# Kernel tuning notes

Hardware: AMD Instinct MI355X
Metric: run time of the kernel (lower is better)

Reference implementation:

```python
import jax, jax.numpy as jnp
import numpy as np

D_MODEL = 1024
NUM_HEADS = 16
HEAD_DIM = D_MODEL // NUM_HEADS
THETA = 10000.0


def _rope(x):
    # x: [B, H, S, Dk]; interleaved even/odd rotation as in the torch module
    *_, seq_len, d_k = x.shape
    d = d_k // 2
    inv_freq = 1.0 / (THETA ** (2.0 * jnp.arange(d, dtype=jnp.float32) / d_k))
    pos = jnp.arange(seq_len, dtype=jnp.float32)
    angles = pos[:, None] * inv_freq[None, :]  # [S, d]
    cos = jnp.cos(angles)
    sin = jnp.sin(angles)
    x_even = x[..., 0::2]
    x_odd = x[..., 1::2]
    rot_even = x_even * cos - x_odd * sin
    rot_odd = x_even * sin + x_odd * cos
    return jnp.stack([rot_even, rot_odd], axis=-1).reshape(x.shape)


def setup_inputs() -> dict:
    key = jax.random.key(0)
    ks = jax.random.split(key, 5)
    B, S = 4, 2048
    x = jax.random.normal(ks[0], (B, S, D_MODEL), dtype=jnp.float32)
    q_w = jax.random.uniform(ks[1], (D_MODEL, D_MODEL), dtype=jnp.float32)
    k_w = jax.random.uniform(ks[2], (D_MODEL, D_MODEL), dtype=jnp.float32)
    v_w = jax.random.uniform(ks[3], (D_MODEL, D_MODEL), dtype=jnp.float32)
    o_w = jax.random.uniform(ks[4], (D_MODEL, D_MODEL), dtype=jnp.float32)
    return {"x": x, "q_w": q_w, "k_w": k_w, "v_w": v_w, "o_w": o_w}


def reference(x, q_w, k_w, v_w, o_w):
    B, S, _ = x.shape
    def split_heads(t):
        return t.reshape(B, S, NUM_HEADS, HEAD_DIM).transpose(0, 2, 1, 3)  # [B,H,S,Dk]
    Q = split_heads(x @ q_w.T)
    K = split_heads(x @ k_w.T)
    V = split_heads(x @ v_w.T)
    Q = _rope(Q)
    K = _rope(K)
    scale = 1.0 / jnp.sqrt(jnp.float32(HEAD_DIM))
    scores = jnp.einsum('bhqd,bhkd->bhqk', Q, K) * scale  # [B,H,S,S]
    causal = jnp.tril(jnp.ones((S, S), dtype=bool))
    scores = jnp.where(causal[None, None], scores, -jnp.inf)
    attn = jax.nn.softmax(scores, axis=-1)
    out = jnp.einsum('bhqk,bhkd->bhqd', attn, V)  # [B,H,S,Dk]
    out = out.transpose(0, 2, 1, 3).reshape(B, S, D_MODEL)
    return out @ o_w.T
```

## Files before the change

### kernel.cpp

```cpp
#include <hip/hip_runtime.h>
#include <hip/hip_bf16.h>
#include <cstdint>
#include <cstddef>

#define D_MODEL   1024
#define NUM_HEADS 16
#define HEAD_DIM  64
#define SEQ       2048
#define BATCH     4
#define BH        (BATCH*NUM_HEADS)
#define MROWS     (BATCH*SEQ)

typedef _Float16 half8  __attribute__((ext_vector_type(8)));
typedef _Float16 half4v __attribute__((ext_vector_type(4)));
typedef float    floatx4 __attribute__((ext_vector_type(4)));

__device__ inline void gld_lds16(const void* g, void* l) {
    __builtin_amdgcn_global_load_lds(
        (__attribute__((address_space(1))) void*)g,
        (__attribute__((address_space(3))) void*)l,
        16, 0, 0);
}

__global__ void rope_table(float2* __restrict__ tab) {
    const int i = blockIdx.x * blockDim.x + threadIdx.x;
    const int p = i & 31, s = i >> 5;
    const double inv = pow(10000.0, -(double)p / 32.0);
    const double ang = (double)s * inv;
    tab[i] = make_float2((float)cos(ang), (float)sin(ang));
}

__global__ void f32_split_f16(const float* __restrict__ in,
                              _Float16* __restrict__ hi,
                              _Float16* __restrict__ lo, int n4) {
    int i = blockIdx.x * blockDim.x + threadIdx.x;
    if (i >= n4) return;
    float4 v = ((const float4*)in)[i];
    half4v h = { (_Float16)v.x, (_Float16)v.y, (_Float16)v.z, (_Float16)v.w };
    half4v l = { (_Float16)(v.x - (float)h.x), (_Float16)(v.y - (float)h.y),
                 (_Float16)(v.z - (float)h.z), (_Float16)(v.w - (float)h.w) };
    ((half4v*)hi)[i] = h;
    ((half4v*)lo)[i] = l;
}

__global__ void conv_weights(const float* __restrict__ qw, const float* __restrict__ kw,
                             const float* __restrict__ vw, const float* __restrict__ ow,
                             _Float16* __restrict__ qwh, _Float16* __restrict__ qwl,
                             _Float16* __restrict__ kwh, _Float16* __restrict__ kwl,
                             _Float16* __restrict__ vwh, _Float16* __restrict__ owh) {
    const int i = blockIdx.x * blockDim.x + threadIdx.x;
    const int which = i >> 18;
    const int j = i & 262143;
    const float4 v = ((const float4*)(which == 0 ? qw : which == 1 ? kw :
                                      which == 2 ? vw : ow))[j];
    half4v h = { (_Float16)v.x, (_Float16)v.y, (_Float16)v.z, (_Float16)v.w };
    if (which < 2) {
        half4v l = { (_Float16)(v.x - (float)h.x), (_Float16)(v.y - (float)h.y),
                     (_Float16)(v.z - (float)h.z), (_Float16)(v.w - (float)h.w) };
        ((half4v*)(which ? kwh : qwh))[j] = h;
        ((half4v*)(which ? kwl : qwl))[j] = l;
    } else {
        ((half4v*)(which == 2 ? vwh : owh))[j] = h;
    }
}

__global__ __launch_bounds__(256)
void gemm_bt(const _Float16* __restrict__ A, const _Float16* __restrict__ B,
             float* __restrict__ Cout, int M, int N, int K) {
    __shared__ _Float16 AB[2][2][128*32];

    const int nb  = N >> 7;
    const int nwg = gridDim.x;
    int lb = blockIdx.x;
    if ((nwg & 7) == 0)
        lb = (blockIdx.x & 7) * (nwg >> 3) + (blockIdx.x >> 3);
    const int bx = lb % nb;
    const int by = lb / nb;
    const int m0 = by << 7, n0 = bx << 7;

    const int t    = threadIdx.x;
    const int w    = t >> 6;
    const int lane = t & 63;
    const int r    = lane & 15;
    const int quad = lane >> 4;
    const int wm   = (w >> 1) << 6;
    const int wn   = (w & 1) << 6;

    const int srow = lane >> 2;
    const int scol = (lane & 3) << 3;

    floatx4 acc[4][4];
    #pragma unroll
    for (int i = 0; i < 4; i++)
        #pragma unroll
        for (int j = 0; j < 4; j++)
            acc[i][j] = (floatx4){0.f, 0.f, 0.f, 0.f};

    auto stageAB = [&](int buf, int kk) {
        #pragma unroll
        for (int p = 0; p < 2; ++p) {
            const int rbase = p*64 + w*16;
            gld_lds16(&A[(size_t)(m0 + rbase + srow)*K + kk + scol], &AB[buf][0][rbase*32]);
            gld_lds16(&B[(size_t)(n0 + rbase + srow)*K + kk + scol], &AB[buf][1][rbase*32]);
        }
    };

    stageAB(0, 0);
    int cur = 0;
    for (int k0 = 0; k0 < K; k0 += 32) {
        __syncthreads();
        if (k0 + 32 < K) stageAB(cur ^ 1, k0 + 32);

        const _Float16* As = AB[cur][0];
        const _Float16* Bs = AB[cur][1];
        half8 af[4], bf[4];
        #pragma unroll
        for (int i = 0; i < 4; i++)
            af[i] = *(const half8*)&As[(wm + i*16 + r)*32 + quad*8];
        #pragma unroll
        for (int j = 0; j < 4; j++)
            bf[j] = *(const half8*)&Bs[(wn + j*16 + r)*32 + quad*8];

        #pragma unroll
        for (int i = 0; i < 4; i++)
            #pragma unroll
            for (int j = 0; j < 4; j++)
                acc[i][j] = __builtin_amdgcn_mfma_f32_16x16x32_f16(
                                af[i], bf[j], acc[i][j], 0, 0, 0);
        cur ^= 1;
    }

    #pragma unroll
    for (int i = 0; i < 4; i++)
        #pragma unroll
        for (int j = 0; j < 4; j++)
            #pragma unroll
            for (int v = 0; v < 4; v++) {
                const int m = m0 + wm + i*16 + quad*4 + v;
                const int n = n0 + wn + j*16 + r;
                Cout[(size_t)m*N + n] = acc[i][j][v];
            }
}

__global__ __launch_bounds__(256)
void gemm_qkv(const _Float16* __restrict__ Axh, const _Float16* __restrict__ Axl,
              const _Float16* __restrict__ qwh, const _Float16* __restrict__ qwl,
              const _Float16* __restrict__ kwh, const _Float16* __restrict__ kwl,
              const _Float16* __restrict__ vwh,
              _Float16* __restrict__ Qhi, _Float16* __restrict__ Qlo,
              _Float16* __restrict__ Khi, _Float16* __restrict__ Klo,
              _Float16* __restrict__ Vt,  const float2* __restrict__ tab) {
    __shared__ _Float16 smem[2][4][4096];

    const int lb  = (blockIdx.x & 7) * 192 + (blockIdx.x >> 3);
    const int bx  = lb % 24;
    const int by  = lb / 24;
    const int wt  = bx >> 3;
    const int n0  = (bx & 7) << 7;
    const int m0  = by << 7;

    const _Float16* Bh = (wt == 0) ? qwh : (wt == 1) ? kwh : vwh;
    const _Float16* Bl = (wt == 0) ? qwl : kwl;

    const int t    = threadIdx.x;
    const int w    = t >> 6;
    const int lane = t & 63;
    const int r    = lane & 15;
    const int quad = lane >> 4;
    const int wm   = (w >> 1) << 6;
    const int wn   = (w & 1) << 6;

    const int srow = lane >> 2;
    const int scol = (lane & 3) << 3;

    floatx4 acc[4][4];
    #pragma unroll
    for (int i = 0; i < 4; i++)
        #pragma unroll
        for (int j = 0; j < 4; j++)
            acc[i][j] = (floatx4){0.f, 0.f, 0.f, 0.f};

    auto stage_k = [&](int buf, int kk) {
        #pragma unroll
        for (int p = 0; p < 2; ++p) {
            const int rbase = p*64 + w*16;
            const size_t ga = (size_t)(m0 + rbase + srow)*1024 + kk + scol;
            const size_t gb = (size_t)(n0 + rbase + srow)*1024 + kk + scol;
            gld_lds16(&Axh[ga], &smem[buf][0][rbase*32]);
            gld_lds16(&Bh [gb], &smem[buf][2][rbase*32]);
            if (wt < 2) {
                gld_lds16(&Axl[ga], &smem[buf][1][rbase*32]);
                gld_lds16(&Bl [gb], &smem[buf][3][rbase*32]);
            }
        }
    };

    stage_k(0, 0);
    int cur = 0;
    for (int k0 = 0; k0 < 1024; k0 += 32) {
        __syncthreads();
        if (k0 + 32 < 1024) stage_k(cur ^ 1, k0 + 32);

        const _Float16* Ash = smem[cur][0];
        const _Float16* Asl = smem[cur][1];
        const _Float16* Bsh = smem[cur][2];
        const _Float16* Bsl = smem[cur][3];

        half8 ah[4], bh[4], al[4], bl[4];
        #pragma unroll
        for (int i = 0; i < 4; i++)
            ah[i] = *(const half8*)&Ash[(wm + i*16 + r)*32 + quad*8];
        #pragma unroll
        for (int j = 0; j < 4; j++)
            bh[j] = *(const half8*)&Bsh[(wn + j*16 + r)*32 + quad*8];
        if (wt < 2) {
            #pragma unroll
            for (int i = 0; i < 4; i++)
                al[i] = *(const half8*)&Asl[(wm + i*16 + r)*32 + quad*8];
            #pragma unroll
            for (int j = 0; j < 4; j++)
                bl[j] = *(const half8*)&Bsl[(wn + j*16 + r)*32 + quad*8];
        }

        if (wt < 2) {
            #pragma unroll
            for (int i = 0; i < 4; i++)
                #pragma unroll
                for (int j = 0; j < 4; j++) {
                    acc[i][j] = __builtin_amdgcn_mfma_f32_16x16x32_f16(
                                    ah[i], bh[j], acc[i][j], 0, 0, 0);
                    acc[i][j] = __builtin_amdgcn_mfma_f32_16x16x32_f16(
                                    ah[i], bl[j], acc[i][j], 0, 0, 0);
                    acc[i][j] = __builtin_amdgcn_mfma_f32_16x16x32_f16(
                                    al[i], bh[j], acc[i][j], 0, 0, 0);
                }
        } else {
            #pragma unroll
            for (int i = 0; i < 4; i++)
                #pragma unroll
                for (int j = 0; j < 4; j++)
                    acc[i][j] = __builtin_amdgcn_mfma_f32_16x16x32_f16(
                                    ah[i], bh[j], acc[i][j], 0, 0, 0);
        }
        cur ^= 1;
    }

    __syncthreads();
    float* sc = (float*)&smem[0][0][0] + w*1088;
    const int g  = lane & 7;
    const int rw = lane >> 3;
    const int hh = (n0 + wn) >> 6;

    if (wt < 2) {
        _Float16* Chi = wt ? Khi : Qhi;
        _Float16* Clo = wt ? Klo : Qlo;
        #pragma unroll
        for (int i = 0; i < 4; i++) {
            #pragma unroll
            for (int j = 0; j < 4; j++)
                #pragma unroll
                for (int v = 0; v < 4; v++)
                    sc[(quad*4 + v)*68 + j*16 + r] = acc[i][j][v];
            #pragma unroll
            for (int rg = 0; rg < 2; rg++) {
                const int row = rw + rg*8;
                const int m   = m0 + wm + i*16 + row;
                const int bb  = m >> 11, s_ = m & 2047;
                const float4 va = *(const float4*)&sc[row*68 + g*8];
                const float4 vb = *(const float4*)&sc[row*68 + g*8 + 4];
                const float vv[8] = {va.x, va.y, va.z, va.w,
                                     vb.x, vb.y, vb.z, vb.w};
                half8 hv, lv;
                #pragma unroll
                for (int p2 = 0; p2 < 4; p2++) {
                    const float2 cs = tab[s_*32 + g*4 + p2];
                    const float e0 = vv[2*p2], o0 = vv[2*p2+1];
                    const float re = e0*cs.x - o0*cs.y;
                    const float ro = e0*cs.y + o0*cs.x;
                    const _Float16 rh = (_Float16)re;
                    const _Float16 oh = (_Float16)ro;
                    hv[2*p2]   = rh; lv[2*p2]   = (_Float16)(re - (float)rh);
                    hv[2*p2+1] = oh; lv[2*p2+1] = (_Float16)(ro - (float)oh);
                }
                const size_t idx = ((((size_t)bb*NUM_HEADS + hh)*SEQ + s_) << 6) + g*8;
                *(half8*)&Chi[idx] = hv;
                *(half8*)&Clo[idx] = lv;
            }
        }
    } else {
        const int d = lane;
        #pragma unroll
        for (int i = 0; i < 4; i++) {
            #pragma unroll
            for (int j = 0; j < 4; j++)
                #pragma unroll
                for (int v = 0; v < 4; v++)
                    sc[(quad*4 + v)*68 + j*16 + r] = acc[i][j][v];
            #pragma unroll
            for (int rg = 0; rg < 2; rg++) {
                const int m  = m0 + wm + i*16 + rg*8;
                const int bb = m >> 11, s_ = m & 2047;
                half8 ov;
                #pragma unroll
                for (int rr = 0; rr < 8; rr++)
                    ov[rr] = (_Float16)sc[(rg*8 + rr)*68 + d];
                *(half8*)&Vt[((((size_t)bb*NUM_HEADS + hh)*HEAD_DIM + d) << 11) + s_] = ov;
            }
        }
    }
}

#define PSTR 72
__global__ __launch_bounds__(256)
void flash_attn(const _Float16* __restrict__ Qhi, const _Float16* __restrict__ Qlo,
                const _Float16* __restrict__ Khi, const _Float16* __restrict__ Klo,
                const _Float16* __restrict__ Vt,  _Float16* __restrict__ AO) {
    __shared__ _Float16 SB[2][6][64*32];
    __shared__ _Float16 Pl[4][16*PSTR];

    const int t    = threadIdx.x;
    const int w    = t >> 6;
    const int lane = t & 63;
    const int r    = lane & 15;
    const int quad = lane >> 4;

    const int bx = blockIdx.x;
    const int bh = bx & 63;
    const int qb = 15 - (bx >> 6);
    const int Q0 = qb << 7;
    const int q0a = Q0 + w*16;
    const int q0b = Q0 + 64 + w*16;
    const int b  = bh >> 4, h = bh & 15;

    const _Float16* Qh_ = Qhi + (size_t)bh * SEQ * HEAD_DIM;
    const _Float16* Ql_ = Qlo + (size_t)bh * SEQ * HEAD_DIM;
    const _Float16* Khg = Khi + (size_t)bh * SEQ * HEAD_DIM;
    const _Float16* Klg = Klo + (size_t)bh * SEQ * HEAD_DIM;
    const _Float16* Vtg = Vt  + (size_t)bh * HEAD_DIM * SEQ;

    half8 qh0[2], ql0[2], qh1[2], ql1[2];
    #pragma unroll
    for (int c = 0; c < 2; ++c) {
        qh0[c] = *(const half8*)&Qh_[(size_t)(q0a + r)*64 + c*32 + quad*8];
        ql0[c] = *(const half8*)&Ql_[(size_t)(q0a + r)*64 + c*32 + quad*8];
        qh1[c] = *(const half8*)&Qh_[(size_t)(q0b + r)*64 + c*32 + quad*8];
        ql1[c] = *(const half8*)&Ql_[(size_t)(q0b + r)*64 + c*32 + quad*8];
    }

    floatx4 ot0[4], ot1[4];
    #pragma unroll
    for (int dt = 0; dt < 4; ++dt) {
        ot0[dt] = (floatx4){0.f,0.f,0.f,0.f};
        ot1[dt] = (floatx4){0.f,0.f,0.f,0.f};
    }
    float mi0 = -1e30f, li0 = 0.f, mi1 = -1e30f, li1 = 0.f;

    const int sr = lane >> 2;
    const int sc = (lane & 3) << 3;
    const int rb = w << 4;

    auto stage = [&](int buf, int kt) {
        const int k0  = kt << 6;
        const int row = rb + sr;
        const size_t kr = (size_t)(k0 + row)*64;
        gld_lds16(&Khg[kr +      sc], &SB[buf][0][rb*32]);
        gld_lds16(&Khg[kr + 32 + sc], &SB[buf][1][rb*32]);
        gld_lds16(&Klg[kr +      sc], &SB[buf][2][rb*32]);
        gld_lds16(&Klg[kr + 32 + sc], &SB[buf][3][rb*32]);
        const size_t vr = (size_t)row*SEQ + k0;
        gld_lds16(&Vtg[vr +      sc], &SB[buf][4][rb*32]);
        gld_lds16(&Vtg[vr + 32 + sc], &SB[buf][5][rb*32]);
    };

    const int niter = 2*qb + 2;
    stage(0, 0);
    int cur = 0;

    for (int kt = 0; kt < niter; ++kt) {
        const int k0 = kt << 6;

        __syncthreads();
        if (kt + 1 < niter) stage(cur ^ 1, kt + 1);

        const _Float16* Kh0 = SB[cur][0];
        const _Float16* Kh1 = SB[cur][1];
        const _Float16* Kl0 = SB[cur][2];
        const _Float16* Kl1 = SB[cur][3];
        const _Float16* Vp0 = SB[cur][4];
        const _Float16* Vp1 = SB[cur][5];

        auto group = [&](int q0g, const half8 (&qhg)[2], const half8 (&qlg)[2],
                         floatx4 (&og)[4], float &mig, float &lig, bool domask) {
            float s[16];
            __builtin_amdgcn_s_setprio(1);
            #pragma unroll
            for (int sub = 0; sub < 4; ++sub) {
                floatx4 a = (floatx4){0.f,0.f,0.f,0.f};
                const int fr = (sub*16 + r)*32 + quad*8;
                const half8 kh0 = *(const half8*)&Kh0[fr];
                const half8 kh1 = *(const half8*)&Kh1[fr];
                const half8 kl0 = *(const half8*)&Kl0[fr];
                const half8 kl1 = *(const half8*)&Kl1[fr];
                a = __builtin_amdgcn_mfma_f32_16x16x32_f16(kh0, qhg[0], a, 0, 0, 0);
                a = __builtin_amdgcn_mfma_f32_16x16x32_f16(kh1, qhg[1], a, 0, 0, 0);
                a = __builtin_amdgcn_mfma_f32_16x16x32_f16(kh0, qlg[0], a, 0, 0, 0);
                a = __builtin_amdgcn_mfma_f32_16x16x32_f16(kh1, qlg[1], a, 0, 0, 0);
                a = __builtin_amdgcn_mfma_f32_16x16x32_f16(kl0, qhg[0], a, 0, 0, 0);
                a = __builtin_amdgcn_mfma_f32_16x16x32_f16(kl1, qhg[1], a, 0, 0, 0);
                #pragma unroll
                for (int v = 0; v < 4; ++v) s[sub*4 + v] = a[v] * 0.125f;
            }
            __builtin_amdgcn_s_setprio(0);

            if (domask) {
                #pragma unroll
                for (int sub = 0; sub < 4; ++sub)
                    #pragma unroll
                    for (int v = 0; v < 4; ++v)
                        if (k0 + sub*16 + quad*4 + v > q0g + r)
                            s[sub*4 + v] = -1e30f;
            }

            float tm = s[0];
            #pragma unroll
            for (int i = 1; i < 16; ++i) tm = fmaxf(tm, s[i]);
            tm = fmaxf(tm, __shfl_xor(tm, 16));
            tm = fmaxf(tm, __shfl_xor(tm, 32));
            const float mn = fmaxf(mig, tm);
            const float alpha = __expf(mig - mn);
            mig = mn;
            float rs = 0.f;
            #pragma unroll
            for (int i = 0; i < 16; ++i) { s[i] = __expf(s[i] - mn); rs += s[i]; }
            rs += __shfl_xor(rs, 16);
            rs += __shfl_xor(rs, 32);
            lig = lig*alpha + rs;
            #pragma unroll
            for (int dt = 0; dt < 4; ++dt)
                #pragma unroll
                for (int v = 0; v < 4; ++v) og[dt][v] *= alpha;

            #pragma unroll
            for (int sub = 0; sub < 4; ++sub) {
                half4v pk = { (_Float16)s[sub*4+0], (_Float16)s[sub*4+1],
                              (_Float16)s[sub*4+2], (_Float16)s[sub*4+3] };
                *(half4v*)&Pl[w][r*PSTR + sub*16 + quad*4] = pk;
            }

            __builtin_amdgcn_s_setprio(1);
            #pragma unroll
            for (int c = 0; c < 2; ++c) {
                const half8 pf = *(const half8*)&Pl[w][r*PSTR + c*32 + quad*8];
                const _Float16* Vsc = c ? Vp1 : Vp0;
                #pragma unroll
                for (int dt = 0; dt < 4; ++dt) {
                    const half8 vf = *(const half8*)&Vsc[(dt*16 + r)*32 + quad*8];
                    og[dt] = __builtin_amdgcn_mfma_f32_16x16x32_f16(vf, pf, og[dt], 0, 0, 0);
                }
            }
            __builtin_amdgcn_s_setprio(0);
        };

        if (kt <= 2*qb) group(q0a, qh0, ql0, ot0, mi0, li0, kt == 2*qb);
        group(q0b, qh1, ql1, ot1, mi1, li1, kt == 2*qb + 1);

        cur ^= 1;
    }

    {
        const float inv0 = 1.0f / li0;
        const int q = q0a + r;
        #pragma unroll
        for (int dt = 0; dt < 4; ++dt) {
            half4v o = { (_Float16)(ot0[dt][0]*inv0), (_Float16)(ot0[dt][1]*inv0),
                         (_Float16)(ot0[dt][2]*inv0), (_Float16)(ot0[dt][3]*inv0) };
            *(half4v*)&AO[((size_t)(b*SEQ + q))*D_MODEL + h*HEAD_DIM + dt*16 + quad*4] = o;
        }
    }
    {
        const float inv1 = 1.0f / li1;
        const int q = q0b + r;
        #pragma unroll
        for (int dt = 0; dt < 4; ++dt) {
            half4v o = { (_Float16)(ot1[dt][0]*inv1), (_Float16)(ot1[dt][1]*inv1),
                         (_Float16)(ot1[dt][2]*inv1), (_Float16)(ot1[dt][3]*inv1) };
            *(half4v*)&AO[((size_t)(b*SEQ + q))*D_MODEL + h*HEAD_DIM + dt*16 + quad*4] = o;
        }
    }
}

extern "C" void kernel_launch(void* const* d_in, const int* in_sizes, int n_in,
                              void* d_out, int out_size, void* d_ws, size_t ws_size,
                              hipStream_t stream) {
    const float* x  = (const float*)d_in[0];
    const float* qw = (const float*)d_in[1];
    const float* kw = (const float*)d_in[2];
    const float* vw = (const float*)d_in[3];
    const float* ow = (const float*)d_in[4];
    float* out = (float*)d_out;

    _Float16* xh  = (_Float16*)d_ws;
    _Float16* xl  = xh  + (size_t)MROWS * D_MODEL;
    _Float16* qwh = xl  + (size_t)MROWS * D_MODEL;
    _Float16* qwl = qwh + (size_t)D_MODEL * D_MODEL;
    _Float16* kwh = qwl + (size_t)D_MODEL * D_MODEL;
    _Float16* kwl = kwh + (size_t)D_MODEL * D_MODEL;
    _Float16* vwh = kwl + (size_t)D_MODEL * D_MODEL;
    _Float16* owh = vwh + (size_t)D_MODEL * D_MODEL;
    _Float16* Qhi = owh + (size_t)D_MODEL * D_MODEL;
    _Float16* Qlo = Qhi + (size_t)MROWS * D_MODEL;
    _Float16* Khi = Qlo + (size_t)MROWS * D_MODEL;
    _Float16* Klo = Khi + (size_t)MROWS * D_MODEL;
    _Float16* Vt  = Klo + (size_t)MROWS * D_MODEL;
    _Float16* AO  = Vt  + (size_t)MROWS * D_MODEL;
    float2*   tab = (float2*)(AO + (size_t)MROWS * D_MODEL);

    rope_table<<<(SEQ*32)/256, 256, 0, stream>>>(tab);

    const int nx4 = MROWS * D_MODEL / 4;
    f32_split_f16<<<nx4/256, 256, 0, stream>>>(x, xh, xl, nx4);
    conv_weights<<<(4*262144)/256, 256, 0, stream>>>(qw, kw, vw, ow,
                                                     qwh, qwl, kwh, kwl, vwh, owh);

    gemm_qkv<<<64*24, 256, 0, stream>>>(xh, xl, qwh, qwl, kwh, kwl, vwh,
                                        Qhi, Qlo, Khi, Klo, Vt, tab);

    flash_attn<<<BH * (SEQ/128), 256, 0, stream>>>(Qhi, Qlo, Khi, Klo, Vt, AO);

    gemm_bt<<<(MROWS/128)*(D_MODEL/128), 256, 0, stream>>>(AO, owh, out,
                                                           MROWS, D_MODEL, D_MODEL);
}
```

Measured before the change: 379.2 us.

## Stage K/V through registers into padded LDS to avoid bank conflicts

Replaces the direct global-to-LDS async loads with register-staged loads issued before compute and written to LDS after compute. This lets the shared tiles use a padded row stride of 40 halves instead of 32, which the direct-to-LDS path could not express. The padding targets LDS bank conflicts on the K and V fragment reads feeding the MFMAs. In exchange it adds register pressure and extra LDS write instructions. The write to the other buffer happens after compute in the same iteration, relying on the next loop-top barrier for ordering.

```diff
diff --git a/kernel.cpp b/kernel.cpp
--- a/kernel.cpp
+++ b/kernel.cpp
@@ -311,11 +311,12 @@
 }
 
 #define PSTR 72
+#define KSTR 40
 __global__ __launch_bounds__(256)
 void flash_attn(const _Float16* __restrict__ Qhi, const _Float16* __restrict__ Qlo,
                 const _Float16* __restrict__ Khi, const _Float16* __restrict__ Klo,
                 const _Float16* __restrict__ Vt,  _Float16* __restrict__ AO) {
-    __shared__ _Float16 SB[2][6][64*32];
+    __shared__ _Float16 SB[2][6][64*KSTR];
     __shared__ _Float16 Pl[4][16*PSTR];
 
     const int t    = threadIdx.x;
@@ -358,29 +359,36 @@
     const int sr = lane >> 2;
     const int sc = (lane & 3) << 3;
     const int rb = w << 4;
-
-    auto stage = [&](int buf, int kt) {
-        const int k0  = kt << 6;
-        const int row = rb + sr;
-        const size_t kr = (size_t)(k0 + row)*64;
-        gld_lds16(&Khg[kr +      sc], &SB[buf][0][rb*32]);
-        gld_lds16(&Khg[kr + 32 + sc], &SB[buf][1][rb*32]);
-        gld_lds16(&Klg[kr +      sc], &SB[buf][2][rb*32]);
-        gld_lds16(&Klg[kr + 32 + sc], &SB[buf][3][rb*32]);
-        const size_t vr = (size_t)row*SEQ + k0;
-        gld_lds16(&Vtg[vr +      sc], &SB[buf][4][rb*32]);
-        gld_lds16(&Vtg[vr + 32 + sc], &SB[buf][5][rb*32]);
+    const int srow = rb + sr;
+
+    half8 rg[6];
+    auto stage_load = [&](int kt) {
+        const int k0 = kt << 6;
+        const size_t kr = (size_t)(k0 + srow)*64;
+        rg[0] = *(const half8*)&Khg[kr +      sc];
+        rg[1] = *(const half8*)&Khg[kr + 32 + sc];
+        rg[2] = *(const half8*)&Klg[kr +      sc];
+        rg[3] = *(const half8*)&Klg[kr + 32 + sc];
+        const size_t vr = (size_t)srow*SEQ + k0;
+        rg[4] = *(const half8*)&Vtg[vr +      sc];
+        rg[5] = *(const half8*)&Vtg[vr + 32 + sc];
     };
+    auto stage_write = [&](int buf) {
+        const int o = srow*KSTR + sc;
+        #pragma unroll
+        for (int p = 0; p < 6; ++p)
+            *(half8*)&SB[buf][p][o] = rg[p];
+    };
 
     const int niter = 2*qb + 2;
-    stage(0, 0);
+    stage_load(0); stage_write(0);
     int cur = 0;
 
     for (int kt = 0; kt < niter; ++kt) {
         const int k0 = kt << 6;
 
         __syncthreads();
-        if (kt + 1 < niter) stage(cur ^ 1, kt + 1);
+        if (kt + 1 < niter) stage_load(kt + 1);
 
         const _Float16* Kh0 = SB[cur][0];
         const _Float16* Kh1 = SB[cur][1];
@@ -396,7 +404,7 @@
             #pragma unroll
             for (int sub = 0; sub < 4; ++sub) {
                 floatx4 a = (floatx4){0.f,0.f,0.f,0.f};
-                const int fr = (sub*16 + r)*32 + quad*8;
+                const int fr = (sub*16 + r)*KSTR + quad*8;
                 const half8 kh0 = *(const half8*)&Kh0[fr];
                 const half8 kh1 = *(const half8*)&Kh1[fr];
                 const half8 kl0 = *(const half8*)&Kl0[fr];
@@ -454,7 +462,7 @@
                 const _Float16* Vsc = c ? Vp1 : Vp0;
                 #pragma unroll
                 for (int dt = 0; dt < 4; ++dt) {
-                    const half8 vf = *(const half8*)&Vsc[(dt*16 + r)*32 + quad*8];
+                    const half8 vf = *(const half8*)&Vsc[(dt*16 + r)*KSTR + quad*8];
                     og[dt] = __builtin_amdgcn_mfma_f32_16x16x32_f16(vf, pf, og[dt], 0, 0, 0);
                 }
             }
@@ -463,6 +471,8 @@
 
         if (kt <= 2*qb) group(q0a, qh0, ql0, ot0, mi0, li0, kt == 2*qb);
         group(q0b, qh1, ql1, ot1, mi1, li1, kt == 2*qb + 1);
+
+        if (kt + 1 < niter) stage_write(cur ^ 1);
 
         cur ^= 1;
     }
```

Measured after the change: 370.2 us (median of 2 runs). 1.02x faster.
